# Kernel tuning notes

Hardware: AMD Instinct MI355X
Metric: run time of the kernel (lower is better)

Reference implementation:

```python
import jax, jax.numpy as jnp
import numpy as np

N = 100000
F = 256
H = 128
C = 64
E = 1600000

def spmm(rows, cols, vals, h):
    # sparse [N,N] @ dense [N,D] via gather + segment-sum
    return jax.ops.segment_sum(vals[:, None] * h[cols], rows, num_segments=N)

def graph_conv(x, W, rows, cols, vals, b=None):
    # GraphConv: support = x @ W; out = adj @ support (+ bias)
    out = spmm(rows, cols, vals, x @ W)
    if b is not None:
        out = out + b
    return out

def setup_inputs() -> dict:
    key = jax.random.key(0)
    ks = jax.random.split(key, 20)
    d = {}
    d['x'] = jax.random.normal(ks[0], (N, F), dtype=jnp.float32)
    for i, name in enumerate(['mid', 'low', 'high']):
        d[name + '_rows'] = jax.random.randint(ks[1 + 3 * i], (E,), 0, N, dtype=jnp.int64 if jax.config.jax_enable_x64 else jnp.int32)
        d[name + '_cols'] = jax.random.randint(ks[2 + 3 * i], (E,), 0, N, dtype=jnp.int64 if jax.config.jax_enable_x64 else jnp.int32)
        d[name + '_vals'] = jax.random.uniform(ks[3 + 3 * i], (E,), dtype=jnp.float32) * 0.1
    s = lambda k, a, b_: jax.random.normal(k, (a, b_), dtype=jnp.float32) * (1.0 / np.sqrt(a))
    d['W_hid'] = s(ks[10], F, H)          # hidden_layers[0], no bias
    d['W_out'] = s(ks[11], H, C)          # out_layer
    d['b_out'] = jnp.zeros((C,), jnp.float32)
    d['W_low'] = s(ks[12], F, H)          # addHid_layer, no bias
    d['W_low_out'] = s(ks[13], H, C)      # addOut_layer
    d['b_low_out'] = jnp.zeros((C,), jnp.float32)
    d['W_high'] = s(ks[14], F, H)         # addHid_layer_HIGH, no bias
    d['W_high_out'] = s(ks[15], H, C)     # addOut_layer_HIGH
    d['b_high_out'] = jnp.zeros((C,), jnp.float32)
    d['gate2'] = jnp.array([0.5], jnp.float32)
    return d

def reference(x, mid_rows, mid_cols, mid_vals, low_rows, low_cols, low_vals,
              high_rows, high_cols, high_vals, W_hid, W_out, b_out,
              W_low, W_low_out, b_low_out, W_high, W_high_out, b_high_out, gate2):
    # dropout is identity at inference
    h = jax.nn.relu(graph_conv(x, W_hid, mid_rows, mid_cols, mid_vals))
    h = graph_conv(h, W_out, mid_rows, mid_cols, mid_vals, b_out)
    x2 = jax.nn.relu(graph_conv(x, W_low, low_rows, low_cols, low_vals))
    xh = jax.nn.relu(graph_conv(x, W_high, high_rows, high_cols, high_vals))
    x2 = graph_conv(x2, W_low_out, low_rows, low_cols, low_vals, b_low_out)
    xh = graph_conv(xh, W_high_out, high_rows, high_cols, high_vals, b_high_out)
    x_final = gate2 * h + (1.0 - gate2) * (x2 + xh)
    return jax.nn.log_softmax(x_final, axis=-1)
```

## Files before the change

kernel.cpp:

```cpp
#include <hip/hip_runtime.h>
#include <math.h>

#define NNODES 100000
#define NEDGES 1600000
#define FEAT 256
#define HID 128
#define NCLS 64
#define RPB 512
#define NBG 196
#define NB3 (3 * NBG)
#define CAP 8832
#define SC_CHUNK 8192
#define SC_THREADS 1024

typedef __attribute__((ext_vector_type(8))) short bf16x8;
typedef __attribute__((ext_vector_type(4))) float f32x4;
typedef __attribute__((ext_vector_type(2))) float f32x2;

__device__ __forceinline__ float bf2f(unsigned int u16) {
  union { unsigned int i; float f; } c; c.i = u16 << 16; return c.f;
}
__device__ __forceinline__ unsigned short f2bf(float f) {
  union { float f; unsigned int i; } c; c.f = f;
  unsigned int u = c.i;
  return (unsigned short)((u + 0x7fffu + ((u >> 16) & 1u)) >> 16);
}

__device__ __forceinline__ void fma8(const uint4 u, const f32x2 vv, f32x2* a) {
  f32x2 p0, p1, p2, p3;
  p0.x = __uint_as_float(u.x << 16); p0.y = __uint_as_float(u.x & 0xffff0000u);
  p1.x = __uint_as_float(u.y << 16); p1.y = __uint_as_float(u.y & 0xffff0000u);
  p2.x = __uint_as_float(u.z << 16); p2.y = __uint_as_float(u.z & 0xffff0000u);
  p3.x = __uint_as_float(u.w << 16); p3.y = __uint_as_float(u.w & 0xffff0000u);
  a[0] += p0 * vv; a[1] += p1 * vv; a[2] += p2 * vv; a[3] += p3 * vv;
}

__global__ __launch_bounds__(256) void k_bhist(const int* __restrict__ r0,
                                               const int* __restrict__ r1,
                                               const int* __restrict__ r2,
                                               int* __restrict__ bhist) {
  __shared__ int h[NBG];
  int g = blockIdx.y;
  const int* rr = (g == 0) ? r0 : (g == 1 ? r1 : r2);
  int tid = threadIdx.x;
  for (int i = tid; i < NBG; i += 256) h[i] = 0;
  __syncthreads();
  int base = blockIdx.x * 4096;
#pragma unroll
  for (int k = 0; k < 16; k++) {
    int e = base + k * 256 + tid;
    if (e < NEDGES) atomicAdd(&h[rr[e] >> 9], 1);
  }
  __syncthreads();
  for (int i = tid; i < NBG; i += 256)
    if (h[i]) atomicAdd(&bhist[g * NBG + i], h[i]);
}

__global__ __launch_bounds__(1024) void k_bscan(const int* __restrict__ bhist,
                                                int* __restrict__ boff) {
  __shared__ int sd[2][1024];
  int tid = threadIdx.x;
  int v = (tid < NB3) ? bhist[tid] : 0;
  sd[0][tid] = v;
  __syncthreads();
  int cur = 0;
  for (int off = 1; off < 1024; off <<= 1) {
    int nv = sd[cur][tid];
    if (tid >= off) nv += sd[cur][tid - off];
    sd[cur ^ 1][tid] = nv;
    __syncthreads();
    cur ^= 1;
  }
  int incl = sd[cur][tid];
  if (tid < NB3) boff[tid] = incl - v;
  if (tid == NB3 - 1) boff[NB3] = incl;
}

__global__ __launch_bounds__(SC_THREADS) void k_bucket_scatter(
    const int* __restrict__ r0, const int* __restrict__ r1, const int* __restrict__ r2,
    const int* __restrict__ c0, const int* __restrict__ c1, const int* __restrict__ c2,
    const float* __restrict__ v0, const float* __restrict__ v1, const float* __restrict__ v2,
    int* __restrict__ gcur, int2* __restrict__ edges) {
  __shared__ int2 stage[SC_CHUNK];
  __shared__ unsigned char bid[SC_CHUNK];
  __shared__ int hist[NBG];
  __shared__ int lbase[NBG];
  __shared__ int gstart[NBG];
  __shared__ int cur[NBG];
  __shared__ int sd[2][256];
  int g = blockIdx.y;
  const int*   rr = (g == 0) ? r0 : (g == 1 ? r1 : r2);
  const int*   cc = (g == 0) ? c0 : (g == 1 ? c1 : c2);
  const float* vv = (g == 0) ? v0 : (g == 1 ? v1 : v2);
  int tid = threadIdx.x;
  int base = blockIdx.x * SC_CHUNK;
  int cnt_blk = NEDGES - base;
  if (cnt_blk > SC_CHUNK) cnt_blk = SC_CHUNK;

  for (int i = tid; i < NBG; i += SC_THREADS) hist[i] = 0;
  __syncthreads();

  int rowv[SC_CHUNK / SC_THREADS];
  int colv[SC_CHUNK / SC_THREADS];
  float valv[SC_CHUNK / SC_THREADS];
#pragma unroll
  for (int k = 0; k < SC_CHUNK / SC_THREADS; k++) {
    int e = base + k * SC_THREADS + tid;
    bool ok = e < NEDGES;
    rowv[k] = ok ? rr[e] : -1;
    colv[k] = ok ? cc[e] : 0;
    valv[k] = ok ? vv[e] : 0.f;
    if (ok) atomicAdd(&hist[rowv[k] >> 9], 1);
  }
  __syncthreads();

  if (tid < 256) sd[0][tid] = (tid < NBG) ? hist[tid] : 0;
  __syncthreads();
  int c = 0;
  for (int off = 1; off < 256; off <<= 1) {
    if (tid < 256) {
      int nv = sd[c][tid];
      if (tid >= off) nv += sd[c][tid - off];
      sd[c ^ 1][tid] = nv;
    }
    __syncthreads();
    c ^= 1;
  }
  if (tid < NBG) {
    int cn = hist[tid];
    int excl = sd[c][tid] - cn;
    lbase[tid] = excl;
    cur[tid] = excl;
    gstart[tid] = cn ? atomicAdd(&gcur[g * NBG + tid], cn) : 0;
  }
  __syncthreads();

#pragma unroll
  for (int k = 0; k < SC_CHUNK / SC_THREADS; k++) {
    if (rowv[k] >= 0) {
      int b = rowv[k] >> 9;
      int p = atomicAdd(&cur[b], 1);
      stage[p] = make_int2(((rowv[k] & (RPB - 1)) << 17) | colv[k], __float_as_int(valv[k]));
      bid[p] = (unsigned char)b;
    }
  }
  __syncthreads();

  for (int i = tid; i < cnt_blk; i += SC_THREADS) {
    int b = bid[i];
    int dst = gstart[b] + (i - lbase[b]);
    edges[dst] = stage[i];
  }
}

__global__ __launch_bounds__(512) void k_bucket_sort(const int* __restrict__ boff,
                                                     int2* __restrict__ edges,
                                                     int* __restrict__ row_ptr_all) {
  __shared__ int2 stage[CAP];
  __shared__ int hist[RPB];
  __shared__ int sd[2][RPB];
  __shared__ int cur[RPB];
  int g = blockIdx.y, b = blockIdx.x;
  int tid = threadIdx.x;
  int idx = g * NBG + b;
  int base = boff[idx];
  int count = boff[idx + 1] - base;
  if (count > CAP) count = CAP;
  hist[tid] = 0;
  __syncthreads();

  const int KSL = (CAP + 511) / 512;
  int2 ev[KSL];
#pragma unroll
  for (int k = 0; k < KSL; k++) {
    int i = tid + k * 512;
    if (i < count) {
      ev[k] = edges[base + i];
      atomicAdd(&hist[ev[k].x >> 17], 1);
    }
  }
  __syncthreads();

  int v = hist[tid];
  sd[0][tid] = v;
  __syncthreads();
  int c2 = 0;
  for (int off = 1; off < 512; off <<= 1) {
    int nv = sd[c2][tid];
    if (tid >= off) nv += sd[c2][tid - off];
    sd[c2 ^ 1][tid] = nv;
    __syncthreads();
    c2 ^= 1;
  }
  int excl = sd[c2][tid] - v;
  int row = b * RPB + tid;
  if (row <= NNODES) row_ptr_all[g * (NNODES + 1) + row] = base + excl;
  cur[tid] = excl;
  __syncthreads();

#pragma unroll
  for (int k = 0; k < KSL; k++) {
    int i = tid + k * 512;
    if (i < count) {
      int lr = ev[k].x >> 17;
      int p = atomicAdd(&cur[lr], 1);
      stage[p] = make_int2(ev[k].x & 0x1FFFF, ev[k].y);
    }
  }
  __syncthreads();

  for (int i = tid; i < count; i += 512) edges[base + i] = stage[i];
}

__global__ __launch_bounds__(256) void k_convert_bf16(const float* __restrict__ src,
                                                      unsigned short* __restrict__ dst,
                                                      int n4) {
  int i = blockIdx.x * blockDim.x + threadIdx.x;
  if (i < n4) {
    float4 v = ((const float4*)src)[i];
    ushort4 o;
    o.x = f2bf(v.x); o.y = f2bf(v.y); o.z = f2bf(v.z); o.w = f2bf(v.w);
    ((ushort4*)dst)[i] = o;
  }
}

__global__ __launch_bounds__(256) void k_transpose3(const float* __restrict__ s0,
                                                    const float* __restrict__ s1,
                                                    const float* __restrict__ s2,
                                                    unsigned short* __restrict__ d0,
                                                    unsigned short* __restrict__ d1,
                                                    unsigned short* __restrict__ d2,
                                                    int K, int N) {
  int g = blockIdx.y;
  const float* src = (g == 0) ? s0 : (g == 1 ? s1 : s2);
  unsigned short* dst = (g == 0) ? d0 : (g == 1 ? d1 : d2);
  int idx = blockIdx.x * 256 + threadIdx.x;
  if (idx < K * N) {
    int k = idx / N, n = idx % N;
    dst[(size_t)n * K + k] = f2bf(src[idx]);
  }
}

__global__ __launch_bounds__(256) void k_gemm1_b(const unsigned short* __restrict__ A,
                                                 const unsigned short* __restrict__ WtA,
                                                 unsigned short* __restrict__ C3, int M) {
  int bxy = blockIdx.x;
  int g = bxy % 3;
  int bx = bxy / 3;
  const unsigned short* Wt = WtA + (size_t)g * HID * FEAT;
  unsigned short* C = C3 + (size_t)g * M * HID;
  int tid = threadIdx.x;
  int wave = tid >> 6, lane = tid & 63;
  int quad = lane >> 4, r = lane & 15;
  int m0 = bx * 128 + wave * 32;
  int ra0 = m0 + r;      if (ra0 >= M) ra0 = 0;
  int ra1 = m0 + 16 + r; if (ra1 >= M) ra1 = 0;
  const unsigned short* pa0 = A + (size_t)ra0 * FEAT + quad * 8;
  const unsigned short* pa1 = A + (size_t)ra1 * FEAT + quad * 8;
  f32x4 acc[2][8];
#pragma unroll
  for (int i = 0; i < 2; i++)
#pragma unroll
    for (int j = 0; j < 8; j++) acc[i][j] = (f32x4){0.f, 0.f, 0.f, 0.f};
  for (int k0 = 0; k0 < FEAT; k0 += 32) {
    bf16x8 a0 = *(const bf16x8*)(pa0 + k0);
    bf16x8 a1 = *(const bf16x8*)(pa1 + k0);
#pragma unroll
    for (int nt = 0; nt < 8; nt++) {
      bf16x8 b = *(const bf16x8*)(Wt + (size_t)(nt * 16 + r) * FEAT + k0 + quad * 8);
      acc[0][nt] = __builtin_amdgcn_mfma_f32_16x16x32_bf16(a0, b, acc[0][nt], 0, 0, 0);
      acc[1][nt] = __builtin_amdgcn_mfma_f32_16x16x32_bf16(a1, b, acc[1][nt], 0, 0, 0);
    }
  }
#pragma unroll
  for (int t = 0; t < 2; t++)
#pragma unroll
    for (int reg = 0; reg < 4; reg++) {
      int row = m0 + t * 16 + quad * 4 + reg;
      if (row < M) {
#pragma unroll
        for (int nt = 0; nt < 8; nt++)
          C[(size_t)row * HID + nt * 16 + r] = f2bf(acc[t][nt][reg]);
      }
    }
}

__global__ __launch_bounds__(256) void k_gemm2_b(const unsigned short* __restrict__ A3,
                                                 const unsigned short* __restrict__ WtA,
                                                 unsigned short* __restrict__ C3, int M) {
  int g = blockIdx.y;
  const unsigned short* A = A3 + (size_t)g * M * HID;
  const unsigned short* Wt = WtA + (size_t)g * NCLS * HID;
  unsigned short* C = C3 + (size_t)g * M * NCLS;
  int tid = threadIdx.x;
  int wave = tid >> 6, lane = tid & 63;
  int quad = lane >> 4, r = lane & 15;
  int m0 = blockIdx.x * 128 + wave * 32;
  int ra0 = m0 + r;      if (ra0 >= M) ra0 = 0;
  int ra1 = m0 + 16 + r; if (ra1 >= M) ra1 = 0;
  const unsigned short* pa0 = A + (size_t)ra0 * HID + quad * 8;
  const unsigned short* pa1 = A + (size_t)ra1 * HID + quad * 8;
  f32x4 acc[2][4];
#pragma unroll
  for (int i = 0; i < 2; i++)
#pragma unroll
    for (int j = 0; j < 4; j++) acc[i][j] = (f32x4){0.f, 0.f, 0.f, 0.f};
  for (int k0 = 0; k0 < HID; k0 += 32) {
    bf16x8 a0 = *(const bf16x8*)(pa0 + k0);
    bf16x8 a1 = *(const bf16x8*)(pa1 + k0);
#pragma unroll
    for (int nt = 0; nt < 4; nt++) {
      bf16x8 b = *(const bf16x8*)(Wt + (size_t)(nt * 16 + r) * HID + k0 + quad * 8);
      acc[0][nt] = __builtin_amdgcn_mfma_f32_16x16x32_bf16(a0, b, acc[0][nt], 0, 0, 0);
      acc[1][nt] = __builtin_amdgcn_mfma_f32_16x16x32_bf16(a1, b, acc[1][nt], 0, 0, 0);
    }
  }
#pragma unroll
  for (int t = 0; t < 2; t++)
#pragma unroll
    for (int reg = 0; reg < 4; reg++) {
      int row = m0 + t * 16 + quad * 4 + reg;
      if (row < M) {
#pragma unroll
        for (int nt = 0; nt < 4; nt++)
          C[(size_t)row * NCLS + nt * 16 + r] = f2bf(acc[t][nt][reg]);
      }
    }
}

__global__ __launch_bounds__(256) void k_spmm128_b(const int* __restrict__ rp_all,
                                                   const int2* __restrict__ edges,
                                                   const unsigned short* __restrict__ dense3,
                                                   unsigned short* __restrict__ out3, int n) {
  int g = blockIdx.y;
  const int* rp = rp_all + (size_t)g * (NNODES + 1);
  const unsigned short* dense = dense3 + (size_t)g * NNODES * HID;
  unsigned short* out = out3 + (size_t)g * NNODES * HID;
  int w = (blockIdx.x * blockDim.x + threadIdx.x) >> 6;
  int lane = threadIdx.x & 63;
  if (w >= n) return;
  int grp = lane >> 4;
  int sub = lane & 15;
  int s = rp[w], e = rp[w + 1];
  f32x2 a0[4], a1[4];
#pragma unroll
  for (int q = 0; q < 4; q++) { a0[q] = (f32x2){0.f, 0.f}; a1[q] = (f32x2){0.f, 0.f}; }
  for (int j = s; j < e; j += 8) {
    int e0 = j + grp, e1 = j + 4 + grp;
    bool k0 = e0 < e, k1 = e1 < e;
    int2 d0 = edges[k0 ? e0 : s];
    int2 d1 = edges[k1 ? e1 : s];
    uint4 u0 = *(const uint4*)(dense + (size_t)d0.x * HID + sub * 8);
    uint4 u1 = *(const uint4*)(dense + (size_t)d1.x * HID + sub * 8);
    float f0 = k0 ? __int_as_float(d0.y) : 0.f;
    float f1 = k1 ? __int_as_float(d1.y) : 0.f;
    f32x2 v0; v0.x = f0; v0.y = f0;
    f32x2 v1; v1.x = f1; v1.y = f1;
    fma8(u0, v0, a0);
    fma8(u1, v1, a1);
  }
  unsigned int pk[4];
#pragma unroll
  for (int q = 0; q < 4; q++) {
    float lo = a0[q].x + a1[q].x;
    float hi = a0[q].y + a1[q].y;
    lo += __shfl_xor(lo, 32, 64); lo += __shfl_xor(lo, 16, 64);
    hi += __shfl_xor(hi, 32, 64); hi += __shfl_xor(hi, 16, 64);
    lo = fmaxf(lo, 0.f); hi = fmaxf(hi, 0.f);
    pk[q] = (unsigned int)f2bf(lo) | ((unsigned int)f2bf(hi) << 16);
  }
  if (lane < 16) {
    uint4 o; o.x = pk[0]; o.y = pk[1]; o.z = pk[2]; o.w = pk[3];
    *(uint4*)(out + (size_t)w * HID + sub * 8) = o;
  }
}

__global__ __launch_bounds__(256) void k_spmm64_b(const int* __restrict__ rp_all,
                                                  const int2* __restrict__ edges,
                                                  const unsigned short* __restrict__ dense3,
                                                  const float* __restrict__ b0p,
                                                  const float* __restrict__ b1p,
                                                  const float* __restrict__ b2p,
                                                  const float* __restrict__ gate,
                                                  float* __restrict__ logits3, int n) {
  int g = blockIdx.y;
  const int* rp = rp_all + (size_t)g * (NNODES + 1);
  const unsigned short* dense = dense3 + (size_t)g * NNODES * NCLS;
  const float* bias = (g == 0) ? b0p : (g == 1 ? b1p : b2p);
  float* logits = logits3 + (size_t)g * NNODES * NCLS;
  int w = (blockIdx.x * blockDim.x + threadIdx.x) >> 6;
  int lane = threadIdx.x & 63;
  if (w >= n) return;
  int grp = lane >> 3;
  int sub = lane & 7;
  int s = rp[w], e = rp[w + 1];
  f32x2 a0[4], a1[4];
#pragma unroll
  for (int q = 0; q < 4; q++) { a0[q] = (f32x2){0.f, 0.f}; a1[q] = (f32x2){0.f, 0.f}; }
  for (int j = s; j < e; j += 16) {
    int e0 = j + grp, e1 = j + 8 + grp;
    bool k0 = e0 < e, k1 = e1 < e;
    int2 d0 = edges[k0 ? e0 : s];
    int2 d1 = edges[k1 ? e1 : s];
    uint4 u0 = *(const uint4*)(dense + (size_t)d0.x * NCLS + sub * 8);
    uint4 u1 = *(const uint4*)(dense + (size_t)d1.x * NCLS + sub * 8);
    float f0 = k0 ? __int_as_float(d0.y) : 0.f;
    float f1 = k1 ? __int_as_float(d1.y) : 0.f;
    f32x2 v0; v0.x = f0; v0.y = f0;
    f32x2 v1; v1.x = f1; v1.y = f1;
    fma8(u0, v0, a0);
    fma8(u1, v1, a1);
  }
  float gv = gate[0];
  float scale = (g == 0) ? gv : (1.0f - gv);
  float vc[8];
#pragma unroll
  for (int q = 0; q < 4; q++) {
    float lo = a0[q].x + a1[q].x;
    float hi = a0[q].y + a1[q].y;
    lo += __shfl_xor(lo, 32, 64); lo += __shfl_xor(lo, 16, 64); lo += __shfl_xor(lo, 8, 64);
    hi += __shfl_xor(hi, 32, 64); hi += __shfl_xor(hi, 16, 64); hi += __shfl_xor(hi, 8, 64);
    vc[2 * q] = lo; vc[2 * q + 1] = hi;
  }
  if (grp == 0) {
    float4 b0 = *(const float4*)(bias + sub * 8);
    float4 b1 = *(const float4*)(bias + sub * 8 + 4);
    size_t o = (size_t)w * NCLS + sub * 8;
    *(float4*)(logits + o) = make_float4(scale * (vc[0] + b0.x), scale * (vc[1] + b0.y),
                                         scale * (vc[2] + b0.z), scale * (vc[3] + b0.w));
    *(float4*)(logits + o + 4) = make_float4(scale * (vc[4] + b1.x), scale * (vc[5] + b1.y),
                                             scale * (vc[6] + b1.z), scale * (vc[7] + b1.w));
  }
}

__global__ __launch_bounds__(256) void k_final(const float* __restrict__ l3,
                                               float* __restrict__ outp, int n) {
  int t = blockIdx.x * 256 + threadIdx.x;
  int w = t >> 3, sub = t & 7;
  if (w >= n) return;
  size_t o = (size_t)w * NCLS + sub * 8;
  const float* p0 = l3 + o;
  const float* p1 = l3 + (size_t)NNODES * NCLS + o;
  const float* p2 = l3 + (size_t)2 * NNODES * NCLS + o;
  float4 x0 = *(const float4*)p0, x1 = *(const float4*)(p0 + 4);
  float4 y0 = *(const float4*)p1, y1 = *(const float4*)(p1 + 4);
  float4 z0 = *(const float4*)p2, z1 = *(const float4*)(p2 + 4);
  float v[8];
  v[0] = x0.x + y0.x + z0.x; v[1] = x0.y + y0.y + z0.y;
  v[2] = x0.z + y0.z + z0.z; v[3] = x0.w + y0.w + z0.w;
  v[4] = x1.x + y1.x + z1.x; v[5] = x1.y + y1.y + z1.y;
  v[6] = x1.z + y1.z + z1.z; v[7] = x1.w + y1.w + z1.w;
  float m = v[0];
#pragma unroll
  for (int i = 1; i < 8; i++) m = fmaxf(m, v[i]);
  m = fmaxf(m, __shfl_xor(m, 1, 64));
  m = fmaxf(m, __shfl_xor(m, 2, 64));
  m = fmaxf(m, __shfl_xor(m, 4, 64));
  float sum = 0.f;
#pragma unroll
  for (int i = 0; i < 8; i++) sum += expf(v[i] - m);
  sum += __shfl_xor(sum, 1, 64);
  sum += __shfl_xor(sum, 2, 64);
  sum += __shfl_xor(sum, 4, 64);
  float ls = m + logf(sum);
  *(float4*)(outp + o)     = make_float4(v[0] - ls, v[1] - ls, v[2] - ls, v[3] - ls);
  *(float4*)(outp + o + 4) = make_float4(v[4] - ls, v[5] - ls, v[6] - ls, v[7] - ls);
}

extern "C" void kernel_launch(void* const* d_in, const int* in_sizes, int n_in,
                              void* d_out, int out_size, void* d_ws, size_t ws_size,
                              hipStream_t stream) {
  (void)in_sizes; (void)n_in; (void)out_size; (void)ws_size;
  const float* x = (const float*)d_in[0];
  const int*   rows[3]   = {(const int*)d_in[1], (const int*)d_in[4], (const int*)d_in[7]};
  const int*   colsIn[3] = {(const int*)d_in[2], (const int*)d_in[5], (const int*)d_in[8]};
  const float* valsIn[3] = {(const float*)d_in[3], (const float*)d_in[6], (const float*)d_in[9]};
  const float* Whid[3] = {(const float*)d_in[10], (const float*)d_in[13], (const float*)d_in[16]};
  const float* Wout[3] = {(const float*)d_in[11], (const float*)d_in[14], (const float*)d_in[17]};
  const float* bout[3] = {(const float*)d_in[12], (const float*)d_in[15], (const float*)d_in[18]};
  const float* gate = (const float*)d_in[19];
  float* out = (float*)d_out;

  const int N = NNODES, E = NEDGES;
  size_t off = 0;
  auto ws = [&](size_t bytes) {
    void* p = (char*)d_ws + off;
    off += (bytes + 255) & ~(size_t)255;
    return p;
  };
  unsigned short* R1 = (unsigned short*)ws((size_t)3 * N * HID * 2);
  unsigned short* x_bf = R1;
  unsigned short* h13  = R1;
  float*          logits3 = (float*)R1;
  unsigned short* hsup3 = (unsigned short*)ws((size_t)3 * N * HID * 2);
  unsigned short* Wt1a = (unsigned short*)ws((size_t)3 * HID * FEAT * 2);
  unsigned short* Wt2a = (unsigned short*)ws((size_t)3 * NCLS * HID * 2);
  int2* edges   = (int2*)ws((size_t)3 * E * 8);
  int*  rp_all  = (int*) ws((size_t)3 * (N + 1) * 4);
  int*  bhist   = (int*) ws(NB3 * 4);
  int*  boff    = (int*) ws((NB3 + 1) * 4);
  int*  gcur    = (int*) ws(NB3 * 4);

  dim3 b256(256);
  dim3 gRows3((N + 3) / 4, 3);
  int nbGemm = (N + 127) / 128;

  k_convert_bf16<<<(N * FEAT / 4 + 255) / 256, b256, 0, stream>>>(x, x_bf, N * FEAT / 4);
  k_transpose3<<<dim3((FEAT * HID + 255) / 256, 3), b256, 0, stream>>>(
      Whid[0], Whid[1], Whid[2], Wt1a, Wt1a + (size_t)HID * FEAT, Wt1a + (size_t)2 * HID * FEAT,
      FEAT, HID);
  k_transpose3<<<dim3((HID * NCLS + 255) / 256, 3), b256, 0, stream>>>(
      Wout[0], Wout[1], Wout[2], Wt2a, Wt2a + (size_t)NCLS * HID, Wt2a + (size_t)2 * NCLS * HID,
      HID, NCLS);

  hipMemsetAsync(bhist, 0, NB3 * 4, stream);
  k_bhist<<<dim3((E + 4095) / 4096, 3), b256, 0, stream>>>(rows[0], rows[1], rows[2], bhist);
  k_bscan<<<1, 1024, 0, stream>>>(bhist, boff);
  hipMemcpyAsync(gcur, boff, NB3 * 4, hipMemcpyDeviceToDevice, stream);
  k_bucket_scatter<<<dim3((E + SC_CHUNK - 1) / SC_CHUNK, 3), dim3(SC_THREADS), 0, stream>>>(
      rows[0], rows[1], rows[2], colsIn[0], colsIn[1], colsIn[2],
      valsIn[0], valsIn[1], valsIn[2], gcur, edges);
  k_bucket_sort<<<dim3(NBG, 3), 512, 0, stream>>>(boff, edges, rp_all);

  k_gemm1_b<<<dim3(3 * nbGemm), b256, 0, stream>>>(x_bf, Wt1a, hsup3, N);
  k_spmm128_b<<<gRows3, b256, 0, stream>>>(rp_all, edges, hsup3, h13, N);
  k_gemm2_b<<<dim3(nbGemm, 3), b256, 0, stream>>>(h13, Wt2a, hsup3, N);
  k_spmm64_b<<<gRows3, b256, 0, stream>>>(rp_all, edges, hsup3, bout[0], bout[1], bout[2],
                                          gate, logits3, N);
  k_final<<<(N * 8 + 255) / 256, b256, 0, stream>>>(logits3, out, N);
}
```

Measured before the change: 727.6 us.

## Compute 128-wide SpMM with MFMA over 16-row edge groups

Replaces the per-row wave gather-FMA SpMM for the hidden layer with a kernel where each wave handles 16 consecutive rows. It gathers 32 neighbor feature rows at a time into LDS and builds a sparse 16x32 bf16 coefficient matrix (row id encoded in edge high bits) to feed MFMA 16x16x32. The bucket sort now packs the local row index into the column field, and the 64-wide SpMM masks it off. The FMA work moves onto matrix cores, but edge values get rounded to bf16 and LDS staging plus sync overhead is added per 32 edges.

```diff
diff --git a/kernel.cpp b/kernel.cpp
--- a/kernel.cpp
+++ b/kernel.cpp
@@ -12,6 +12,9 @@
 #define CAP 8832
 #define SC_CHUNK 8192
 #define SC_THREADS 1024
+#define GRP 16
+#define NGRP (NNODES / GRP)
+#define SLOTP 33
 
 typedef __attribute__((ext_vector_type(8))) short bf16x8;
 typedef __attribute__((ext_vector_type(4))) float f32x4;
@@ -204,7 +207,7 @@
     if (i < count) {
       int lr = ev[k].x >> 17;
       int p = atomicAdd(&cur[lr], 1);
-      stage[p] = make_int2(ev[k].x & 0x1FFFF, ev[k].y);
+      stage[p] = make_int2(((lr & 15) << 17) | (ev[k].x & 0x1FFFF), ev[k].y);
     }
   }
   __syncthreads();
@@ -328,51 +331,80 @@
     }
 }
 
-__global__ __launch_bounds__(256) void k_spmm128_b(const int* __restrict__ rp_all,
-                                                   const int2* __restrict__ edges,
-                                                   const unsigned short* __restrict__ dense3,
-                                                   unsigned short* __restrict__ out3, int n) {
+__global__ __launch_bounds__(256) void k_spmm128_mfma(const int* __restrict__ rp_all,
+                                                      const int2* __restrict__ edges,
+                                                      const unsigned short* __restrict__ dense3,
+                                                      unsigned short* __restrict__ out3) {
+  __shared__ unsigned int Lw_all[4][64 * SLOTP];
   int g = blockIdx.y;
   const int* rp = rp_all + (size_t)g * (NNODES + 1);
   const unsigned short* dense = dense3 + (size_t)g * NNODES * HID;
   unsigned short* out = out3 + (size_t)g * NNODES * HID;
-  int w = (blockIdx.x * blockDim.x + threadIdx.x) >> 6;
-  int lane = threadIdx.x & 63;
-  if (w >= n) return;
-  int grp = lane >> 4;
-  int sub = lane & 15;
-  int s = rp[w], e = rp[w + 1];
-  f32x2 a0[4], a1[4];
-#pragma unroll
-  for (int q = 0; q < 4; q++) { a0[q] = (f32x2){0.f, 0.f}; a1[q] = (f32x2){0.f, 0.f}; }
-  for (int j = s; j < e; j += 8) {
-    int e0 = j + grp, e1 = j + 4 + grp;
-    bool k0 = e0 < e, k1 = e1 < e;
-    int2 d0 = edges[k0 ? e0 : s];
-    int2 d1 = edges[k1 ? e1 : s];
-    uint4 u0 = *(const uint4*)(dense + (size_t)d0.x * HID + sub * 8);
-    uint4 u1 = *(const uint4*)(dense + (size_t)d1.x * HID + sub * 8);
-    float f0 = k0 ? __int_as_float(d0.y) : 0.f;
-    float f1 = k1 ? __int_as_float(d1.y) : 0.f;
-    f32x2 v0; v0.x = f0; v0.y = f0;
-    f32x2 v1; v1.x = f1; v1.y = f1;
-    fma8(u0, v0, a0);
-    fma8(u1, v1, a1);
-  }
-  unsigned int pk[4];
-#pragma unroll
-  for (int q = 0; q < 4; q++) {
-    float lo = a0[q].x + a1[q].x;
-    float hi = a0[q].y + a1[q].y;
-    lo += __shfl_xor(lo, 32, 64); lo += __shfl_xor(lo, 16, 64);
-    hi += __shfl_xor(hi, 32, 64); hi += __shfl_xor(hi, 16, 64);
-    lo = fmaxf(lo, 0.f); hi = fmaxf(hi, 0.f);
-    pk[q] = (unsigned int)f2bf(lo) | ((unsigned int)f2bf(hi) << 16);
-  }
-  if (lane < 16) {
-    uint4 o; o.x = pk[0]; o.y = pk[1]; o.z = pk[2]; o.w = pk[3];
-    *(uint4*)(out + (size_t)w * HID + sub * 8) = o;
-  }
+  int tid = threadIdx.x;
+  int wave = tid >> 6, lane = tid & 63;
+  int q = lane >> 4, n = lane & 15;
+  int grp_id = blockIdx.x * 4 + wave;
+  if (grp_id >= NGRP) return;
+  int r0 = grp_id * GRP;
+  int s = rp[r0], e = rp[r0 + GRP];
+
+  unsigned int* Lw = Lw_all[wave];
+  unsigned int* wbase = Lw + (4 * n) * SLOTP + q;
+  unsigned int bsel = (n & 1) ? 0x07060302u : 0x05040100u;
+
+  f32x4 acc[8];
+#pragma unroll
+  for (int i = 0; i < 8; i++) acc[i] = (f32x4){0.f, 0.f, 0.f, 0.f};
+
+  for (int kb = 0; kb < e - s; kb += 32) {
+    const int2* ep = edges + s + kb;
+#pragma unroll
+    for (int it = 0; it < 8; it++) {
+      int2 ed = ep[it * 4 + q];
+      int col = ed.x & 0x1FFFF;
+      col = (col < NNODES) ? col : 0;
+      uint4 du = *(const uint4*)(dense + (size_t)col * HID + n * 8);
+      unsigned int* wp = wbase + it * 4;
+      wp[0] = du.x; wp[SLOTP] = du.y; wp[2 * SLOTP] = du.z; wp[3 * SLOTP] = du.w;
+    }
+    float fv[8];
+#pragma unroll
+    for (int p = 0; p < 8; p++) {
+      int2 ed = ep[q * 8 + p];
+      bool ok = (kb + q * 8 + p) < (e - s);
+      bool mt = ((((unsigned)ed.x) >> 17) & 15u) == (unsigned)n;
+      fv[p] = (ok && mt) ? __int_as_float(ed.y) : 0.f;
+    }
+    union { unsigned u[4]; bf16x8 v; } A;
+#pragma unroll
+    for (int m = 0; m < 4; m++)
+      A.u[m] = (unsigned)f2bf(fv[2 * m]) | ((unsigned)f2bf(fv[2 * m + 1]) << 16);
+
+    asm volatile("s_waitcnt lgkmcnt(0)" ::: "memory");
+    __builtin_amdgcn_sched_barrier(0);
+
+#pragma unroll
+    for (int nt = 0; nt < 8; nt++) {
+      int fp = nt * 8 + (n >> 1);
+      const unsigned int* rb = Lw + fp * SLOTP + q * 8;
+      union { unsigned u[4]; bf16x8 v; } B;
+#pragma unroll
+      for (int m = 0; m < 4; m++) {
+        unsigned w0 = rb[2 * m];
+        unsigned w1 = rb[2 * m + 1];
+        B.u[m] = __builtin_amdgcn_perm(w1, w0, bsel);
+      }
+      acc[nt] = __builtin_amdgcn_mfma_f32_16x16x32_bf16(A.v, B.v, acc[nt], 0, 0, 0);
+    }
+  }
+
+#pragma unroll
+  for (int nt = 0; nt < 8; nt++)
+#pragma unroll
+    for (int reg = 0; reg < 4; reg++) {
+      int row = r0 + q * 4 + reg;
+      out[(size_t)row * HID + nt * 16 + n] = f2bf(fmaxf(acc[nt][reg], 0.f));
+    }
 }
 
 __global__ __launch_bounds__(256) void k_spmm64_b(const int* __restrict__ rp_all,
@@ -402,8 +434,8 @@
     bool k0 = e0 < e, k1 = e1 < e;
     int2 d0 = edges[k0 ? e0 : s];
     int2 d1 = edges[k1 ? e1 : s];
-    uint4 u0 = *(const uint4*)(dense + (size_t)d0.x * NCLS + sub * 8);
-    uint4 u1 = *(const uint4*)(dense + (size_t)d1.x * NCLS + sub * 8);
+    uint4 u0 = *(const uint4*)(dense + (size_t)(d0.x & 0x1FFFF) * NCLS + sub * 8);
+    uint4 u1 = *(const uint4*)(dense + (size_t)(d1.x & 0x1FFFF) * NCLS + sub * 8);
     float f0 = k0 ? __int_as_float(d0.y) : 0.f;
     float f1 = k1 ? __int_as_float(d1.y) : 0.f;
     f32x2 v0; v0.x = f0; v0.y = f0;
@@ -495,7 +527,7 @@
   unsigned short* hsup3 = (unsigned short*)ws((size_t)3 * N * HID * 2);
   unsigned short* Wt1a = (unsigned short*)ws((size_t)3 * HID * FEAT * 2);
   unsigned short* Wt2a = (unsigned short*)ws((size_t)3 * NCLS * HID * 2);
-  int2* edges   = (int2*)ws((size_t)3 * E * 8);
+  int2* edges   = (int2*)ws(((size_t)3 * E + 64) * 8);
   int*  rp_all  = (int*) ws((size_t)3 * (N + 1) * 4);
   int*  bhist   = (int*) ws(NB3 * 4);
   int*  boff    = (int*) ws((NB3 + 1) * 4);
@@ -523,7 +555,7 @@
   k_bucket_sort<<<dim3(NBG, 3), 512, 0, stream>>>(boff, edges, rp_all);
 
   k_gemm1_b<<<dim3(3 * nbGemm), b256, 0, stream>>>(x_bf, Wt1a, hsup3, N);
-  k_spmm128_b<<<gRows3, b256, 0, stream>>>(rp_all, edges, hsup3, h13, N);
+  k_spmm128_mfma<<<dim3((NGRP + 3) / 4, 3), b256, 0, stream>>>(rp_all, edges, hsup3, h13);
   k_gemm2_b<<<dim3(nbGemm, 3), b256, 0, stream>>>(h13, Wt2a, hsup3, N);
   k_spmm64_b<<<gRows3, b256, 0, stream>>>(rp_all, edges, hsup3, bout[0], bout[1], bout[2],
                                           gate, logits3, N);
```

After: 855.8 us. 1.18x slower.

## Use fixed-capacity buckets, drop histogram pass, fuse final spmm with log-softmax

Applied to the files above, without the earlier changes.

Replaces the histogram and scan prepass with fixed-capacity per-bucket edge slots sized CAP, so the bucket scatter counts with atomics directly and separate row start/end arrays replace the row pointer. The 128-wide SpMM now keeps four independent gathers in flight per iteration instead of two. The three 64-wide SpMMs, the gated sum and log-softmax are fused into one kernel, which removes the logits round trip through memory and two launches. Edges beyond CAP per bucket are silently dropped, and the workspace grows to hold padded buckets.

```diff
diff --git a/kernel.cpp b/kernel.cpp
--- a/kernel.cpp
+++ b/kernel.cpp
@@ -33,47 +33,6 @@
   p2.x = __uint_as_float(u.z << 16); p2.y = __uint_as_float(u.z & 0xffff0000u);
   p3.x = __uint_as_float(u.w << 16); p3.y = __uint_as_float(u.w & 0xffff0000u);
   a[0] += p0 * vv; a[1] += p1 * vv; a[2] += p2 * vv; a[3] += p3 * vv;
-}
-
-__global__ __launch_bounds__(256) void k_bhist(const int* __restrict__ r0,
-                                               const int* __restrict__ r1,
-                                               const int* __restrict__ r2,
-                                               int* __restrict__ bhist) {
-  __shared__ int h[NBG];
-  int g = blockIdx.y;
-  const int* rr = (g == 0) ? r0 : (g == 1 ? r1 : r2);
-  int tid = threadIdx.x;
-  for (int i = tid; i < NBG; i += 256) h[i] = 0;
-  __syncthreads();
-  int base = blockIdx.x * 4096;
-#pragma unroll
-  for (int k = 0; k < 16; k++) {
-    int e = base + k * 256 + tid;
-    if (e < NEDGES) atomicAdd(&h[rr[e] >> 9], 1);
-  }
-  __syncthreads();
-  for (int i = tid; i < NBG; i += 256)
-    if (h[i]) atomicAdd(&bhist[g * NBG + i], h[i]);
-}
-
-__global__ __launch_bounds__(1024) void k_bscan(const int* __restrict__ bhist,
-                                                int* __restrict__ boff) {
-  __shared__ int sd[2][1024];
-  int tid = threadIdx.x;
-  int v = (tid < NB3) ? bhist[tid] : 0;
-  sd[0][tid] = v;
-  __syncthreads();
-  int cur = 0;
-  for (int off = 1; off < 1024; off <<= 1) {
-    int nv = sd[cur][tid];
-    if (tid >= off) nv += sd[cur][tid - off];
-    sd[cur ^ 1][tid] = nv;
-    __syncthreads();
-    cur ^= 1;
-  }
-  int incl = sd[cur][tid];
-  if (tid < NB3) boff[tid] = incl - v;
-  if (tid == NB3 - 1) boff[NB3] = incl;
 }
 
 __global__ __launch_bounds__(SC_THREADS) void k_bucket_scatter(
@@ -148,14 +107,16 @@
 
   for (int i = tid; i < cnt_blk; i += SC_THREADS) {
     int b = bid[i];
-    int dst = gstart[b] + (i - lbase[b]);
-    edges[dst] = stage[i];
-  }
-}
-
-__global__ __launch_bounds__(512) void k_bucket_sort(const int* __restrict__ boff,
+    int pos = gstart[b] + (i - lbase[b]);
+    if (pos < CAP)
+      edges[(size_t)(g * NBG + b) * CAP + pos] = stage[i];
+  }
+}
+
+__global__ __launch_bounds__(512) void k_bucket_sort(const int* __restrict__ gcur,
                                                      int2* __restrict__ edges,
-                                                     int* __restrict__ row_ptr_all) {
+                                                     int* __restrict__ rps_all,
+                                                     int* __restrict__ rpe_all) {
   __shared__ int2 stage[CAP];
   __shared__ int hist[RPB];
   __shared__ int sd[2][RPB];
@@ -163,8 +124,8 @@
   int g = blockIdx.y, b = blockIdx.x;
   int tid = threadIdx.x;
   int idx = g * NBG + b;
-  int base = boff[idx];
-  int count = boff[idx + 1] - base;
+  size_t base = (size_t)idx * CAP;
+  int count = gcur[idx];
   if (count > CAP) count = CAP;
   hist[tid] = 0;
   __syncthreads();
@@ -194,7 +155,10 @@
   }
   int excl = sd[c2][tid] - v;
   int row = b * RPB + tid;
-  if (row <= NNODES) row_ptr_all[g * (NNODES + 1) + row] = base + excl;
+  if (row < NNODES) {
+    rps_all[g * NNODES + row] = (int)base + excl;
+    rpe_all[g * NNODES + row] = (int)base + excl + v;
+  }
   cur[tid] = excl;
   __syncthreads();
 
@@ -328,12 +292,14 @@
     }
 }
 
-__global__ __launch_bounds__(256) void k_spmm128_b(const int* __restrict__ rp_all,
+__global__ __launch_bounds__(256) void k_spmm128_b(const int* __restrict__ rps_all,
+                                                   const int* __restrict__ rpe_all,
                                                    const int2* __restrict__ edges,
                                                    const unsigned short* __restrict__ dense3,
                                                    unsigned short* __restrict__ out3, int n) {
   int g = blockIdx.y;
-  const int* rp = rp_all + (size_t)g * (NNODES + 1);
+  const int* rs = rps_all + (size_t)g * NNODES;
+  const int* re = rpe_all + (size_t)g * NNODES;
   const unsigned short* dense = dense3 + (size_t)g * NNODES * HID;
   unsigned short* out = out3 + (size_t)g * NNODES * HID;
   int w = (blockIdx.x * blockDim.x + threadIdx.x) >> 6;
@@ -341,29 +307,34 @@
   if (w >= n) return;
   int grp = lane >> 4;
   int sub = lane & 15;
-  int s = rp[w], e = rp[w + 1];
-  f32x2 a0[4], a1[4];
-#pragma unroll
-  for (int q = 0; q < 4; q++) { a0[q] = (f32x2){0.f, 0.f}; a1[q] = (f32x2){0.f, 0.f}; }
-  for (int j = s; j < e; j += 8) {
-    int e0 = j + grp, e1 = j + 4 + grp;
-    bool k0 = e0 < e, k1 = e1 < e;
-    int2 d0 = edges[k0 ? e0 : s];
-    int2 d1 = edges[k1 ? e1 : s];
-    uint4 u0 = *(const uint4*)(dense + (size_t)d0.x * HID + sub * 8);
-    uint4 u1 = *(const uint4*)(dense + (size_t)d1.x * HID + sub * 8);
-    float f0 = k0 ? __int_as_float(d0.y) : 0.f;
-    float f1 = k1 ? __int_as_float(d1.y) : 0.f;
-    f32x2 v0; v0.x = f0; v0.y = f0;
-    f32x2 v1; v1.x = f1; v1.y = f1;
-    fma8(u0, v0, a0);
-    fma8(u1, v1, a1);
+  int s = rs[w], e = re[w];
+  f32x2 a[4][4];
+#pragma unroll
+  for (int t = 0; t < 4; t++)
+#pragma unroll
+    for (int q = 0; q < 4; q++) a[t][q] = (f32x2){0.f, 0.f};
+  for (int j = s; j < e; j += 16) {
+    uint4 u[4];
+    float f[4];
+#pragma unroll
+    for (int t = 0; t < 4; t++) {
+      int ej = j + t * 4 + grp;
+      bool ok = ej < e;
+      int2 dd = edges[ok ? ej : s];
+      u[t] = *(const uint4*)(dense + (size_t)dd.x * HID + sub * 8);
+      f[t] = ok ? __int_as_float(dd.y) : 0.f;
+    }
+#pragma unroll
+    for (int t = 0; t < 4; t++) {
+      f32x2 vv; vv.x = f[t]; vv.y = f[t];
+      fma8(u[t], vv, a[t]);
+    }
   }
   unsigned int pk[4];
 #pragma unroll
   for (int q = 0; q < 4; q++) {
-    float lo = a0[q].x + a1[q].x;
-    float hi = a0[q].y + a1[q].y;
+    float lo = (a[0][q].x + a[1][q].x) + (a[2][q].x + a[3][q].x);
+    float hi = (a[0][q].y + a[1][q].y) + (a[2][q].y + a[3][q].y);
     lo += __shfl_xor(lo, 32, 64); lo += __shfl_xor(lo, 16, 64);
     hi += __shfl_xor(hi, 32, 64); hi += __shfl_xor(hi, 16, 64);
     lo = fmaxf(lo, 0.f); hi = fmaxf(hi, 0.f);
@@ -375,96 +346,83 @@
   }
 }
 
-__global__ __launch_bounds__(256) void k_spmm64_b(const int* __restrict__ rp_all,
-                                                  const int2* __restrict__ edges,
-                                                  const unsigned short* __restrict__ dense3,
-                                                  const float* __restrict__ b0p,
-                                                  const float* __restrict__ b1p,
-                                                  const float* __restrict__ b2p,
-                                                  const float* __restrict__ gate,
-                                                  float* __restrict__ logits3, int n) {
-  int g = blockIdx.y;
-  const int* rp = rp_all + (size_t)g * (NNODES + 1);
-  const unsigned short* dense = dense3 + (size_t)g * NNODES * NCLS;
-  const float* bias = (g == 0) ? b0p : (g == 1 ? b1p : b2p);
-  float* logits = logits3 + (size_t)g * NNODES * NCLS;
+__global__ __launch_bounds__(256) void k_spmm64_final(const int* __restrict__ rps_all,
+                                                      const int* __restrict__ rpe_all,
+                                                      const int2* __restrict__ edges,
+                                                      const unsigned short* __restrict__ dense3,
+                                                      const float* __restrict__ b0p,
+                                                      const float* __restrict__ b1p,
+                                                      const float* __restrict__ b2p,
+                                                      const float* __restrict__ gate,
+                                                      float* __restrict__ outp, int n) {
   int w = (blockIdx.x * blockDim.x + threadIdx.x) >> 6;
   int lane = threadIdx.x & 63;
   if (w >= n) return;
   int grp = lane >> 3;
   int sub = lane & 7;
-  int s = rp[w], e = rp[w + 1];
-  f32x2 a0[4], a1[4];
-#pragma unroll
-  for (int q = 0; q < 4; q++) { a0[q] = (f32x2){0.f, 0.f}; a1[q] = (f32x2){0.f, 0.f}; }
-  for (int j = s; j < e; j += 16) {
-    int e0 = j + grp, e1 = j + 8 + grp;
-    bool k0 = e0 < e, k1 = e1 < e;
-    int2 d0 = edges[k0 ? e0 : s];
-    int2 d1 = edges[k1 ? e1 : s];
-    uint4 u0 = *(const uint4*)(dense + (size_t)d0.x * NCLS + sub * 8);
-    uint4 u1 = *(const uint4*)(dense + (size_t)d1.x * NCLS + sub * 8);
-    float f0 = k0 ? __int_as_float(d0.y) : 0.f;
-    float f1 = k1 ? __int_as_float(d1.y) : 0.f;
-    f32x2 v0; v0.x = f0; v0.y = f0;
-    f32x2 v1; v1.x = f1; v1.y = f1;
-    fma8(u0, v0, a0);
-    fma8(u1, v1, a1);
-  }
   float gv = gate[0];
-  float scale = (g == 0) ? gv : (1.0f - gv);
-  float vc[8];
-#pragma unroll
-  for (int q = 0; q < 4; q++) {
-    float lo = a0[q].x + a1[q].x;
-    float hi = a0[q].y + a1[q].y;
-    lo += __shfl_xor(lo, 32, 64); lo += __shfl_xor(lo, 16, 64); lo += __shfl_xor(lo, 8, 64);
-    hi += __shfl_xor(hi, 32, 64); hi += __shfl_xor(hi, 16, 64); hi += __shfl_xor(hi, 8, 64);
-    vc[2 * q] = lo; vc[2 * q + 1] = hi;
-  }
-  if (grp == 0) {
-    float4 b0 = *(const float4*)(bias + sub * 8);
-    float4 b1 = *(const float4*)(bias + sub * 8 + 4);
-    size_t o = (size_t)w * NCLS + sub * 8;
-    *(float4*)(logits + o) = make_float4(scale * (vc[0] + b0.x), scale * (vc[1] + b0.y),
-                                         scale * (vc[2] + b0.z), scale * (vc[3] + b0.w));
-    *(float4*)(logits + o + 4) = make_float4(scale * (vc[4] + b1.x), scale * (vc[5] + b1.y),
-                                             scale * (vc[6] + b1.z), scale * (vc[7] + b1.w));
-  }
-}
-
-__global__ __launch_bounds__(256) void k_final(const float* __restrict__ l3,
-                                               float* __restrict__ outp, int n) {
-  int t = blockIdx.x * 256 + threadIdx.x;
-  int w = t >> 3, sub = t & 7;
-  if (w >= n) return;
-  size_t o = (size_t)w * NCLS + sub * 8;
-  const float* p0 = l3 + o;
-  const float* p1 = l3 + (size_t)NNODES * NCLS + o;
-  const float* p2 = l3 + (size_t)2 * NNODES * NCLS + o;
-  float4 x0 = *(const float4*)p0, x1 = *(const float4*)(p0 + 4);
-  float4 y0 = *(const float4*)p1, y1 = *(const float4*)(p1 + 4);
-  float4 z0 = *(const float4*)p2, z1 = *(const float4*)(p2 + 4);
-  float v[8];
-  v[0] = x0.x + y0.x + z0.x; v[1] = x0.y + y0.y + z0.y;
-  v[2] = x0.z + y0.z + z0.z; v[3] = x0.w + y0.w + z0.w;
-  v[4] = x1.x + y1.x + z1.x; v[5] = x1.y + y1.y + z1.y;
-  v[6] = x1.z + y1.z + z1.z; v[7] = x1.w + y1.w + z1.w;
-  float m = v[0];
-#pragma unroll
-  for (int i = 1; i < 8; i++) m = fmaxf(m, v[i]);
+  float omg = 1.0f - gv;
+  float tot[8];
+  {
+    float4 x0 = *(const float4*)(b0p + sub * 8), x1 = *(const float4*)(b0p + sub * 8 + 4);
+    float4 y0 = *(const float4*)(b1p + sub * 8), y1 = *(const float4*)(b1p + sub * 8 + 4);
+    float4 z0 = *(const float4*)(b2p + sub * 8), z1 = *(const float4*)(b2p + sub * 8 + 4);
+    tot[0] = gv * x0.x + omg * (y0.x + z0.x); tot[1] = gv * x0.y + omg * (y0.y + z0.y);
+    tot[2] = gv * x0.z + omg * (y0.z + z0.z); tot[3] = gv * x0.w + omg * (y0.w + z0.w);
+    tot[4] = gv * x1.x + omg * (y1.x + z1.x); tot[5] = gv * x1.y + omg * (y1.y + z1.y);
+    tot[6] = gv * x1.z + omg * (y1.z + z1.z); tot[7] = gv * x1.w + omg * (y1.w + z1.w);
+  }
+  for (int g = 0; g < 3; g++) {
+    const int* rs = rps_all + (size_t)g * NNODES;
+    const int* re = rpe_all + (size_t)g * NNODES;
+    const unsigned short* dense = dense3 + (size_t)g * NNODES * NCLS;
+    int s = rs[w], e = re[w];
+    f32x2 a0[4], a1[4];
+#pragma unroll
+    for (int q = 0; q < 4; q++) { a0[q] = (f32x2){0.f, 0.f}; a1[q] = (f32x2){0.f, 0.f}; }
+    for (int j = s; j < e; j += 16) {
+      int e0 = j + grp, e1 = j + 8 + grp;
+      bool k0 = e0 < e, k1 = e1 < e;
+      int2 d0 = edges[k0 ? e0 : s];
+      int2 d1 = edges[k1 ? e1 : s];
+      uint4 u0 = *(const uint4*)(dense + (size_t)d0.x * NCLS + sub * 8);
+      uint4 u1 = *(const uint4*)(dense + (size_t)d1.x * NCLS + sub * 8);
+      float f0 = k0 ? __int_as_float(d0.y) : 0.f;
+      float f1 = k1 ? __int_as_float(d1.y) : 0.f;
+      f32x2 v0; v0.x = f0; v0.y = f0;
+      f32x2 v1; v1.x = f1; v1.y = f1;
+      fma8(u0, v0, a0);
+      fma8(u1, v1, a1);
+    }
+    float scale = (g == 0) ? gv : omg;
+#pragma unroll
+    for (int q = 0; q < 4; q++) {
+      float lo = a0[q].x + a1[q].x;
+      float hi = a0[q].y + a1[q].y;
+      lo += __shfl_xor(lo, 32, 64); lo += __shfl_xor(lo, 16, 64); lo += __shfl_xor(lo, 8, 64);
+      hi += __shfl_xor(hi, 32, 64); hi += __shfl_xor(hi, 16, 64); hi += __shfl_xor(hi, 8, 64);
+      tot[2 * q] += scale * lo;
+      tot[2 * q + 1] += scale * hi;
+    }
+  }
+  float m = tot[0];
+#pragma unroll
+  for (int i = 1; i < 8; i++) m = fmaxf(m, tot[i]);
   m = fmaxf(m, __shfl_xor(m, 1, 64));
   m = fmaxf(m, __shfl_xor(m, 2, 64));
   m = fmaxf(m, __shfl_xor(m, 4, 64));
   float sum = 0.f;
 #pragma unroll
-  for (int i = 0; i < 8; i++) sum += expf(v[i] - m);
+  for (int i = 0; i < 8; i++) sum += expf(tot[i] - m);
   sum += __shfl_xor(sum, 1, 64);
   sum += __shfl_xor(sum, 2, 64);
   sum += __shfl_xor(sum, 4, 64);
   float ls = m + logf(sum);
-  *(float4*)(outp + o)     = make_float4(v[0] - ls, v[1] - ls, v[2] - ls, v[3] - ls);
-  *(float4*)(outp + o + 4) = make_float4(v[4] - ls, v[5] - ls, v[6] - ls, v[7] - ls);
+  if (grp == 0) {
+    size_t o = (size_t)w * NCLS + sub * 8;
+    *(float4*)(outp + o)     = make_float4(tot[0] - ls, tot[1] - ls, tot[2] - ls, tot[3] - ls);
+    *(float4*)(outp + o + 4) = make_float4(tot[4] - ls, tot[5] - ls, tot[6] - ls, tot[7] - ls);
+  }
 }
 
 extern "C" void kernel_launch(void* const* d_in, const int* in_sizes, int n_in,
@@ -491,14 +449,12 @@
   unsigned short* R1 = (unsigned short*)ws((size_t)3 * N * HID * 2);
   unsigned short* x_bf = R1;
   unsigned short* h13  = R1;
-  float*          logits3 = (float*)R1;
   unsigned short* hsup3 = (unsigned short*)ws((size_t)3 * N * HID * 2);
   unsigned short* Wt1a = (unsigned short*)ws((size_t)3 * HID * FEAT * 2);
   unsigned short* Wt2a = (unsigned short*)ws((size_t)3 * NCLS * HID * 2);
-  int2* edges   = (int2*)ws((size_t)3 * E * 8);
-  int*  rp_all  = (int*) ws((size_t)3 * (N + 1) * 4);
-  int*  bhist   = (int*) ws(NB3 * 4);
-  int*  boff    = (int*) ws((NB3 + 1) * 4);
+  int2* edges   = (int2*)ws((size_t)NB3 * CAP * 8);
+  int*  rps_all = (int*) ws((size_t)3 * N * 4);
+  int*  rpe_all = (int*) ws((size_t)3 * N * 4);
   int*  gcur    = (int*) ws(NB3 * 4);
 
   dim3 b256(256);
@@ -513,19 +469,15 @@
       Wout[0], Wout[1], Wout[2], Wt2a, Wt2a + (size_t)NCLS * HID, Wt2a + (size_t)2 * NCLS * HID,
       HID, NCLS);
 
-  hipMemsetAsync(bhist, 0, NB3 * 4, stream);
-  k_bhist<<<dim3((E + 4095) / 4096, 3), b256, 0, stream>>>(rows[0], rows[1], rows[2], bhist);
-  k_bscan<<<1, 1024, 0, stream>>>(bhist, boff);
-  hipMemcpyAsync(gcur, boff, NB3 * 4, hipMemcpyDeviceToDevice, stream);
+  hipMemsetAsync(gcur, 0, NB3 * 4, stream);
   k_bucket_scatter<<<dim3((E + SC_CHUNK - 1) / SC_CHUNK, 3), dim3(SC_THREADS), 0, stream>>>(
       rows[0], rows[1], rows[2], colsIn[0], colsIn[1], colsIn[2],
       valsIn[0], valsIn[1], valsIn[2], gcur, edges);
-  k_bucket_sort<<<dim3(NBG, 3), 512, 0, stream>>>(boff, edges, rp_all);
+  k_bucket_sort<<<dim3(NBG, 3), 512, 0, stream>>>(gcur, edges, rps_all, rpe_all);
 
   k_gemm1_b<<<dim3(3 * nbGemm), b256, 0, stream>>>(x_bf, Wt1a, hsup3, N);
-  k_spmm128_b<<<gRows3, b256, 0, stream>>>(rp_all, edges, hsup3, h13, N);
+  k_spmm128_b<<<gRows3, b256, 0, stream>>>(rps_all, rpe_all, edges, hsup3, h13, N);
   k_gemm2_b<<<dim3(nbGemm, 3), b256, 0, stream>>>(h13, Wt2a, hsup3, N);
-  k_spmm64_b<<<gRows3, b256, 0, stream>>>(rp_all, edges, hsup3, bout[0], bout[1], bout[2],
-                                          gate, logits3, N);
-  k_final<<<(N * 8 + 255) / 256, b256, 0, stream>>>(logits3, out, N);
-}
+  k_spmm64_final<<<gRows3.x == 0 ? dim3(1) : dim3((N + 3) / 4), b256, 0, stream>>>(
+      rps_all, rpe_all, edges, hsup3, bout[0], bout[1], bout[2], gate, out, N);
+}
```

Result: slower. 753.0 us (+3.5%).

## Fuse three 64-wide SpMMs with gated combine and log-softmax into one kernel

Applied to the files above, without the earlier changes.

Replaces the per-graph 64-column SpMM kernel and the separate log-softmax kernel with one kernel. Each wavefront walks all three adjacency rows at once, applies the gate and biases in registers, and writes log-softmax output directly. This removes the write and re-read of three float logits arrays (about 77 MB) and one launch, and gives each wave three independent gather streams. In exchange, each wave now processes 8 edges per iteration per graph instead of 16, runs for the longest of the three rows, and uses more registers for three accumulator sets.

```diff
diff --git a/kernel.cpp b/kernel.cpp
--- a/kernel.cpp
+++ b/kernel.cpp
@@ -17,9 +17,6 @@
 typedef __attribute__((ext_vector_type(4))) float f32x4;
 typedef __attribute__((ext_vector_type(2))) float f32x2;
 
-__device__ __forceinline__ float bf2f(unsigned int u16) {
-  union { unsigned int i; float f; } c; c.i = u16 << 16; return c.f;
-}
 __device__ __forceinline__ unsigned short f2bf(float f) {
   union { float f; unsigned int i; } c; c.f = f;
   unsigned int u = c.i;
@@ -375,96 +372,97 @@
   }
 }
 
-__global__ __launch_bounds__(256) void k_spmm64_b(const int* __restrict__ rp_all,
-                                                  const int2* __restrict__ edges,
-                                                  const unsigned short* __restrict__ dense3,
-                                                  const float* __restrict__ b0p,
-                                                  const float* __restrict__ b1p,
-                                                  const float* __restrict__ b2p,
-                                                  const float* __restrict__ gate,
-                                                  float* __restrict__ logits3, int n) {
-  int g = blockIdx.y;
-  const int* rp = rp_all + (size_t)g * (NNODES + 1);
-  const unsigned short* dense = dense3 + (size_t)g * NNODES * NCLS;
-  const float* bias = (g == 0) ? b0p : (g == 1 ? b1p : b2p);
-  float* logits = logits3 + (size_t)g * NNODES * NCLS;
+__global__ __launch_bounds__(256) void k_spmm64_final(const int* __restrict__ rp_all,
+                                                      const int2* __restrict__ edges,
+                                                      const unsigned short* __restrict__ dense3,
+                                                      const float* __restrict__ b0p,
+                                                      const float* __restrict__ b1p,
+                                                      const float* __restrict__ b2p,
+                                                      const float* __restrict__ gate,
+                                                      float* __restrict__ outp, int n) {
   int w = (blockIdx.x * blockDim.x + threadIdx.x) >> 6;
   int lane = threadIdx.x & 63;
   if (w >= n) return;
   int grp = lane >> 3;
   int sub = lane & 7;
-  int s = rp[w], e = rp[w + 1];
-  f32x2 a0[4], a1[4];
-#pragma unroll
-  for (int q = 0; q < 4; q++) { a0[q] = (f32x2){0.f, 0.f}; a1[q] = (f32x2){0.f, 0.f}; }
-  for (int j = s; j < e; j += 16) {
-    int e0 = j + grp, e1 = j + 8 + grp;
-    bool k0 = e0 < e, k1 = e1 < e;
-    int2 d0 = edges[k0 ? e0 : s];
-    int2 d1 = edges[k1 ? e1 : s];
-    uint4 u0 = *(const uint4*)(dense + (size_t)d0.x * NCLS + sub * 8);
-    uint4 u1 = *(const uint4*)(dense + (size_t)d1.x * NCLS + sub * 8);
+  int s[3], e[3];
+#pragma unroll
+  for (int g = 0; g < 3; g++) {
+    s[g] = __builtin_amdgcn_readfirstlane(rp_all[(size_t)g * (NNODES + 1) + w]);
+    e[g] = __builtin_amdgcn_readfirstlane(rp_all[(size_t)g * (NNODES + 1) + w + 1]);
+  }
+  int nit = 0;
+#pragma unroll
+  for (int g = 0; g < 3; g++) {
+    int t = (e[g] - s[g] + 7) >> 3;
+    nit = (t > nit) ? t : nit;
+  }
+  f32x2 ac0[4], ac1[4], ac2[4];
+#pragma unroll
+  for (int q = 0; q < 4; q++) {
+    ac0[q] = (f32x2){0.f, 0.f}; ac1[q] = (f32x2){0.f, 0.f}; ac2[q] = (f32x2){0.f, 0.f};
+  }
+  const unsigned short* d0b = dense3;
+  const unsigned short* d1b = dense3 + (size_t)NNODES * NCLS;
+  const unsigned short* d2b = dense3 + (size_t)2 * NNODES * NCLS;
+  for (int it = 0; it < nit; it++) {
+    int j0 = s[0] + it * 8 + grp, j1 = s[1] + it * 8 + grp, j2 = s[2] + it * 8 + grp;
+    bool k0 = j0 < e[0], k1 = j1 < e[1], k2 = j2 < e[2];
+    int2 d0 = edges[k0 ? j0 : s[0]];
+    int2 d1 = edges[k1 ? j1 : s[1]];
+    int2 d2 = edges[k2 ? j2 : s[2]];
+    uint4 u0 = *(const uint4*)(d0b + (size_t)d0.x * NCLS + sub * 8);
+    uint4 u1 = *(const uint4*)(d1b + (size_t)d1.x * NCLS + sub * 8);
+    uint4 u2 = *(const uint4*)(d2b + (size_t)d2.x * NCLS + sub * 8);
     float f0 = k0 ? __int_as_float(d0.y) : 0.f;
     float f1 = k1 ? __int_as_float(d1.y) : 0.f;
+    float f2 = k2 ? __int_as_float(d2.y) : 0.f;
     f32x2 v0; v0.x = f0; v0.y = f0;
     f32x2 v1; v1.x = f1; v1.y = f1;
-    fma8(u0, v0, a0);
-    fma8(u1, v1, a1);
+    f32x2 v2; v2.x = f2; v2.y = f2;
+    fma8(u0, v0, ac0);
+    fma8(u1, v1, ac1);
+    fma8(u2, v2, ac2);
   }
   float gv = gate[0];
-  float scale = (g == 0) ? gv : (1.0f - gv);
-  float vc[8];
+  float omg = 1.0f - gv;
+  float tot[8];
+  {
+    float4 x0 = *(const float4*)(b0p + sub * 8), x1 = *(const float4*)(b0p + sub * 8 + 4);
+    float4 y0 = *(const float4*)(b1p + sub * 8), y1 = *(const float4*)(b1p + sub * 8 + 4);
+    float4 z0 = *(const float4*)(b2p + sub * 8), z1 = *(const float4*)(b2p + sub * 8 + 4);
+    tot[0] = gv * x0.x + omg * (y0.x + z0.x); tot[1] = gv * x0.y + omg * (y0.y + z0.y);
+    tot[2] = gv * x0.z + omg * (y0.z + z0.z); tot[3] = gv * x0.w + omg * (y0.w + z0.w);
+    tot[4] = gv * x1.x + omg * (y1.x + z1.x); tot[5] = gv * x1.y + omg * (y1.y + z1.y);
+    tot[6] = gv * x1.z + omg * (y1.z + z1.z); tot[7] = gv * x1.w + omg * (y1.w + z1.w);
+  }
 #pragma unroll
   for (int q = 0; q < 4; q++) {
-    float lo = a0[q].x + a1[q].x;
-    float hi = a0[q].y + a1[q].y;
+    float lo = gv * ac0[q].x + omg * (ac1[q].x + ac2[q].x);
+    float hi = gv * ac0[q].y + omg * (ac1[q].y + ac2[q].y);
     lo += __shfl_xor(lo, 32, 64); lo += __shfl_xor(lo, 16, 64); lo += __shfl_xor(lo, 8, 64);
     hi += __shfl_xor(hi, 32, 64); hi += __shfl_xor(hi, 16, 64); hi += __shfl_xor(hi, 8, 64);
-    vc[2 * q] = lo; vc[2 * q + 1] = hi;
-  }
-  if (grp == 0) {
-    float4 b0 = *(const float4*)(bias + sub * 8);
-    float4 b1 = *(const float4*)(bias + sub * 8 + 4);
-    size_t o = (size_t)w * NCLS + sub * 8;
-    *(float4*)(logits + o) = make_float4(scale * (vc[0] + b0.x), scale * (vc[1] + b0.y),
-                                         scale * (vc[2] + b0.z), scale * (vc[3] + b0.w));
-    *(float4*)(logits + o + 4) = make_float4(scale * (vc[4] + b1.x), scale * (vc[5] + b1.y),
-                                             scale * (vc[6] + b1.z), scale * (vc[7] + b1.w));
-  }
-}
-
-__global__ __launch_bounds__(256) void k_final(const float* __restrict__ l3,
-                                               float* __restrict__ outp, int n) {
-  int t = blockIdx.x * 256 + threadIdx.x;
-  int w = t >> 3, sub = t & 7;
-  if (w >= n) return;
-  size_t o = (size_t)w * NCLS + sub * 8;
-  const float* p0 = l3 + o;
-  const float* p1 = l3 + (size_t)NNODES * NCLS + o;
-  const float* p2 = l3 + (size_t)2 * NNODES * NCLS + o;
-  float4 x0 = *(const float4*)p0, x1 = *(const float4*)(p0 + 4);
-  float4 y0 = *(const float4*)p1, y1 = *(const float4*)(p1 + 4);
-  float4 z0 = *(const float4*)p2, z1 = *(const float4*)(p2 + 4);
-  float v[8];
-  v[0] = x0.x + y0.x + z0.x; v[1] = x0.y + y0.y + z0.y;
-  v[2] = x0.z + y0.z + z0.z; v[3] = x0.w + y0.w + z0.w;
-  v[4] = x1.x + y1.x + z1.x; v[5] = x1.y + y1.y + z1.y;
-  v[6] = x1.z + y1.z + z1.z; v[7] = x1.w + y1.w + z1.w;
-  float m = v[0];
-#pragma unroll
-  for (int i = 1; i < 8; i++) m = fmaxf(m, v[i]);
+    tot[2 * q] += lo;
+    tot[2 * q + 1] += hi;
+  }
+  float m = tot[0];
+#pragma unroll
+  for (int i = 1; i < 8; i++) m = fmaxf(m, tot[i]);
   m = fmaxf(m, __shfl_xor(m, 1, 64));
   m = fmaxf(m, __shfl_xor(m, 2, 64));
   m = fmaxf(m, __shfl_xor(m, 4, 64));
   float sum = 0.f;
 #pragma unroll
-  for (int i = 0; i < 8; i++) sum += expf(v[i] - m);
+  for (int i = 0; i < 8; i++) sum += expf(tot[i] - m);
   sum += __shfl_xor(sum, 1, 64);
   sum += __shfl_xor(sum, 2, 64);
   sum += __shfl_xor(sum, 4, 64);
   float ls = m + logf(sum);
-  *(float4*)(outp + o)     = make_float4(v[0] - ls, v[1] - ls, v[2] - ls, v[3] - ls);
-  *(float4*)(outp + o + 4) = make_float4(v[4] - ls, v[5] - ls, v[6] - ls, v[7] - ls);
+  if (grp == 0) {
+    size_t o = (size_t)w * NCLS + sub * 8;
+    *(float4*)(outp + o)     = make_float4(tot[0] - ls, tot[1] - ls, tot[2] - ls, tot[3] - ls);
+    *(float4*)(outp + o + 4) = make_float4(tot[4] - ls, tot[5] - ls, tot[6] - ls, tot[7] - ls);
+  }
 }
 
 extern "C" void kernel_launch(void* const* d_in, const int* in_sizes, int n_in,
@@ -491,11 +489,10 @@
   unsigned short* R1 = (unsigned short*)ws((size_t)3 * N * HID * 2);
   unsigned short* x_bf = R1;
   unsigned short* h13  = R1;
-  float*          logits3 = (float*)R1;
   unsigned short* hsup3 = (unsigned short*)ws((size_t)3 * N * HID * 2);
   unsigned short* Wt1a = (unsigned short*)ws((size_t)3 * HID * FEAT * 2);
   unsigned short* Wt2a = (unsigned short*)ws((size_t)3 * NCLS * HID * 2);
-  int2* edges   = (int2*)ws((size_t)3 * E * 8);
+  int2* edges   = (int2*)ws(((size_t)3 * E + 64) * 8);
   int*  rp_all  = (int*) ws((size_t)3 * (N + 1) * 4);
   int*  bhist   = (int*) ws(NB3 * 4);
   int*  boff    = (int*) ws((NB3 + 1) * 4);
@@ -525,7 +522,6 @@
   k_gemm1_b<<<dim3(3 * nbGemm), b256, 0, stream>>>(x_bf, Wt1a, hsup3, N);
   k_spmm128_b<<<gRows3, b256, 0, stream>>>(rp_all, edges, hsup3, h13, N);
   k_gemm2_b<<<dim3(nbGemm, 3), b256, 0, stream>>>(h13, Wt2a, hsup3, N);
-  k_spmm64_b<<<gRows3, b256, 0, stream>>>(rp_all, edges, hsup3, bout[0], bout[1], bout[2],
-                                          gate, logits3, N);
-  k_final<<<(N * 8 + 255) / 256, b256, 0, stream>>>(logits3, out, N);
-}
+  k_spmm64_final<<<dim3((N + 3) / 4), b256, 0, stream>>>(
+      rp_all, edges, hsup3, bout[0], bout[1], bout[2], gate, out, N);
+}
```

New measurement: 697.5 us. -4.1%, faster.
